# Performance work log

Hardware: AMD Instinct MI355X
Metric: run time of the kernel (lower is better)

The kernel has to match this reference:

```python
import jax, jax.numpy as jnp
import numpy as np

B, T, N = 256, 512, 256
START, STOP = 254, 255


def setup_inputs() -> dict:
    key = jax.random.key(0)
    k1, k2, k3 = jax.random.split(key, 3)
    inputs = jax.random.normal(k1, (B, T, N), dtype=jnp.float32)
    transitions = jax.random.normal(k2, (N, N), dtype=jnp.float32)
    # sentinel rows/cols as in __init__
    transitions = transitions.at[START, :].set(-10000.0).at[:, STOP].set(-10000.0)
    tags = jax.random.randint(k3, (B, T), 0, N, dtype=jnp.int32)
    mask = jnp.ones((B, T), dtype=jnp.int32)
    return {"inputs": inputs, "transitions": transitions, "tags": tags, "mask": mask}


def _input_likelihood(inputs, transitions, fmask):
    # alpha[b, tag]: log-sum over paths ending at tag
    alpha0 = transitions[:, START][None, :] + inputs[:, 0, :]

    def step(alpha, xs):
        emit, m = xs  # emit: (B, N), m: (B,)
        # inner[b, next, prev] = alpha[b, prev] + (emit[b, next] + trans[next, prev]) * mask[b, i-1]
        inner = alpha[:, None, :] + (emit[:, :, None] + transitions[None, :, :]) * m[:, None, None]
        return jax.nn.logsumexp(inner, axis=-1), None

    xs = (jnp.swapaxes(inputs[:, 1:, :], 0, 1), jnp.swapaxes(fmask[:, :-1], 0, 1))
    alpha, _ = jax.lax.scan(step, alpha0, xs)
    stops = alpha + transitions[STOP][None, :]
    return jax.nn.logsumexp(stops, axis=-1)  # (B,)


def _joint_likelihood(inputs, transitions, tags, fmask):
    score = transitions[tags[:, 0], START]  # (B,)
    # transitions[next, prev] * mask[:, i+1], summed over steps
    trans_sc = transitions[tags[:, 1:], tags[:, :-1]] * fmask[:, 1:]
    # inputs[b, i, prev_tag] * mask[:, i]
    emit_sc = jnp.take_along_axis(inputs[:, :-1, :], tags[:, :-1, None], axis=2)[..., 0] * fmask[:, :-1]
    score = score + trans_sc.sum(axis=-1) + emit_sc.sum(axis=-1)
    last_idx = (fmask.sum(axis=-1) - 1.0).astype(jnp.int32)  # (B,)
    last_tags = jnp.take_along_axis(tags, last_idx[:, None], axis=1)[:, 0]
    last_input = jnp.take_along_axis(inputs[:, -1, :], last_tags[:, None], axis=1)[:, 0]
    return score + transitions[STOP, last_tags] + last_input * fmask[:, -1]


def reference(inputs, transitions, tags, mask):
    fmask = mask.astype(jnp.float32)
    log_denominator = _input_likelihood(inputs, transitions, fmask)
    log_numerator = _joint_likelihood(inputs, transitions, tags, fmask)
    return jnp.sum(log_numerator - log_denominator)
```

## Files before the change

### kernel.cpp

```cpp
#include <hip/hip_runtime.h>
#include <hip/hip_bf16.h>
#include <stdint.h>

#define B_    256
#define T_    512
#define N_    256
#define START_ 254
#define STOP_  255
#define GCOLS 16
#define NF    16
#define ND    32
#define LOG2E 1.4426950408889634f
#define LN2   0.6931471805599453f

#define WSB_OFF 65536
#define WCF_OFF 131072
#define WCB_OFF 131328

typedef __attribute__((ext_vector_type(4))) float floatx4;
typedef __attribute__((ext_vector_type(4))) unsigned int uintx4;
typedef __attribute__((ext_vector_type(8))) int v8i;

template<bool X> struct BC { static constexpr bool value = X; };

__device__ __forceinline__ void lds_barrier() {
    asm volatile("s_waitcnt lgkmcnt(0)\n\ts_barrier" ::: "memory");
}

__device__ __forceinline__ int pk_fp8x4(float a, float b, float c, float d) {
    int r = __builtin_amdgcn_cvt_pk_fp8_f32(a, b, 0, false);
    return __builtin_amdgcn_cvt_pk_fp8_f32(c, d, r, true);
}
__device__ __forceinline__ int pk_bf8x4(float a, float b, float c, float d) {
    int r = __builtin_amdgcn_cvt_pk_bf8_f32(a, b, 0, false);
    return __builtin_amdgcn_cvt_pk_bf8_f32(c, d, r, true);
}

struct DenomShared {
    alignas(16) char  V[2][4096];
    alignas(16) float mbuf[GCOLS * 36];
    alignas(16) float sbuf[GCOLS * 20];
    int flag;
};

template<bool ISF>
__device__ __forceinline__ void denom_path(
    DenomShared& sh, const float* __restrict__ inputs,
    const float* __restrict__ trans, const int* __restrict__ mask,
    float* __restrict__ ws, int blkLocal)
{
    const int tid = threadIdx.x;
    const int w = tid >> 6;
    const int l = tid & 63;
    const int q = l >> 4;
    const int b = l & 15;
    const int bg = blkLocal * GCOLS + b;
    const int j0 = 32 * w + 4 * q;
    const int S = ISF ? 256 : 255;
    const int scl = 0x7F7F7F7F;

    auto EIDX = [](int s) { return ISF ? s : (511 - s); };
    auto MIDX = [](int s) { return ISF ? (s - 1) : (511 - s); };

    int wa[2];
    #pragma unroll
    for (int mt = 0; mt < 2; ++mt)
        wa[mt] = ((((2 * w + mt) >> 3) * 2 + mt) << 10)
               + ((w & 3) << 8) + (b << 4) + (q << 2);
    const int rbase = l << 4;

    v8i afrag[2][2];
    #pragma unroll
    for (int mt = 0; mt < 2; ++mt) {
        const int row = 32 * w + 16 * mt + b;
        #pragma unroll
        for (int c = 0; c < 2; ++c) {
            v8i a;
            #pragma unroll
            for (int g8 = 0; g8 < 8; ++g8) {
                float e[4];
                if (ISF) {
                    floatx4 t = *(const floatx4*)(trans + row * N_ + c * 128 + q * 32 + 4 * g8);
                    #pragma unroll
                    for (int ii = 0; ii < 4; ++ii)
                        e[ii] = __builtin_amdgcn_exp2f(t[ii] * LOG2E);
                } else {
                    #pragma unroll
                    for (int ii = 0; ii < 4; ++ii) {
                        const int k = c * 128 + q * 32 + 4 * g8 + ii;
                        e[ii] = __builtin_amdgcn_exp2f(trans[k * N_ + row] * LOG2E);
                    }
                }
                a[g8] = pk_fp8x4(e[0], e[1], e[2], e[3]);
            }
            afrag[mt][c] = a;
        }
    }

    {
        const int* mrow = mask + blkLocal * GCOLS * T_;
        bool hd = false;
        #pragma unroll
        for (int i = 0; i < GCOLS * T_ / 512; ++i)
            hd |= (mrow[tid + 512 * i] == 0);
        if (tid == 0) sh.flag = 0;
        __syncthreads();
        if (__any(hd) && l == 0) atomicOr(&sh.flag, 1);
        __syncthreads();
    }
    const bool anyDead = (sh.flag != 0);

    const float* emitp = inputs + (size_t)bg * T_ * N_;
    const int*   maskp = mask + bg * T_;
    float C = 0.f;
    float u[2][4];

    if (ISF) {
        #pragma unroll
        for (int mt = 0; mt < 2; ++mt) {
            floatx4 em = *(const floatx4*)(emitp + j0 + 16 * mt);
            #pragma unroll
            for (int r = 0; r < 4; ++r) {
                const int j = j0 + 16 * mt + r;
                u[mt][r] = __builtin_amdgcn_exp2f((trans[j * N_ + START_] + em[r]) * LOG2E);
            }
        }
    } else {
        #pragma unroll
        for (int mt = 0; mt < 2; ++mt) {
            floatx4 st = *(const floatx4*)(trans + STOP_ * N_ + j0 + 16 * mt);
            #pragma unroll
            for (int r = 0; r < 4; ++r)
                u[mt][r] = __builtin_amdgcn_exp2f(st[r] * LOG2E);
        }
    }
    {
        float mx = u[0][0], sm = 0.f;
        #pragma unroll
        for (int mt = 0; mt < 2; ++mt)
            #pragma unroll
            for (int r = 0; r < 4; ++r) { mx = fmaxf(mx, u[mt][r]); sm += u[mt][r]; }
        sh.mbuf[b * 36 + w * 4 + q] = mx;
        sm += __shfl_xor(sm, 32, 64);
        if (l < 32) sh.sbuf[b * 20 + w * 2 + q] = sm;

        float xpi[2][4] = {{1.f,1.f,1.f,1.f},{1.f,1.f,1.f,1.f}};
        if (!ISF) {
            #pragma unroll
            for (int mt = 0; mt < 2; ++mt) {
                floatx4 e = *(const floatx4*)(emitp + (size_t)511 * N_ + j0 + 16 * mt);
                #pragma unroll
                for (int r = 0; r < 4; ++r)
                    xpi[mt][r] = __builtin_amdgcn_exp2f(e[r] * LOG2E);
            }
        }
        #pragma unroll
        for (int mt = 0; mt < 2; ++mt)
            *(int*)(sh.V[0] + wa[mt]) =
                pk_bf8x4(u[mt][0] * xpi[mt][0], u[mt][1] * xpi[mt][1],
                         u[mt][2] * xpi[mt][2], u[mt][3] * xpi[mt][3]);
    }

    auto run = [&](auto fastc) {
        constexpr bool FAST = decltype(fastc)::value;
        floatx4 ebuf[2][2];
        float   mrot[2] = {1.f, 1.f};
        ebuf[0][0] = *(const floatx4*)(emitp + (size_t)EIDX(1) * N_ + j0);
        ebuf[0][1] = *(const floatx4*)(emitp + (size_t)EIDX(1) * N_ + j0 + 16);
        ebuf[1][0] = *(const floatx4*)(emitp + (size_t)EIDX(2) * N_ + j0);
        ebuf[1][1] = *(const floatx4*)(emitp + (size_t)EIDX(2) * N_ + j0 + 16);
        if (!FAST) {
            mrot[0] = (float)maskp[MIDX(1)];
            mrot[1] = (float)maskp[MIDX(2)];
        }
        lds_barrier();

        auto body = [&](int s, int pr, int cur) {
            const int sp = (s + 2 <= S) ? s + 2 : S;
            floatx4 eC0 = *(const floatx4*)(emitp + (size_t)EIDX(sp) * N_ + j0);
            floatx4 eC1 = *(const floatx4*)(emitp + (size_t)EIDX(sp) * N_ + j0 + 16);
            float mC = 1.f;
            if (!FAST) mC = (float)maskp[MIDX(sp)];

            const char* vb = sh.V[pr];
            v8i bfrag[2];
            #pragma unroll
            for (int c = 0; c < 2; ++c) {
                uintx4 r0 = *(const uintx4*)(vb + (c << 11) + rbase);
                uintx4 r1 = *(const uintx4*)(vb + (c << 11) + 1024 + rbase);
                v8i bf;
                bf[0] = r0[0]; bf[1] = r0[1]; bf[2] = r0[2]; bf[3] = r0[3];
                bf[4] = r1[0]; bf[5] = r1[1]; bf[6] = r1[2]; bf[7] = r1[3];
                bfrag[c] = bf;
            }

            const float* mb = &sh.mbuf[b * 36];
            float cmax;
            {
                floatx4 mm[8];
                #pragma unroll
                for (int i = 0; i < 8; ++i) mm[i] = *(const floatx4*)(mb + 4 * i);
                floatx4 mv = mm[0];
                #pragma unroll
                for (int i = 1; i < 8; ++i)
                    #pragma unroll
                    for (int r = 0; r < 4; ++r) mv[r] = fmaxf(mv[r], mm[i][r]);
                cmax = fmaxf(fmaxf(mv[0], mv[1]), fmaxf(mv[2], mv[3]));
            }
            const uint32_t cb = __builtin_bit_cast(uint32_t, cmax);
            const int eb = (int)((cb >> 23) & 0xFFu);
            const float rs = __builtin_bit_cast(float, (uint32_t)(249 - eb) << 23);
            const float dCf = (float)(122 - eb);

            float xpv[2][4];
            #pragma unroll
            for (int r = 0; r < 4; ++r) {
                if (ISF) {
                    xpv[0][r] = __builtin_amdgcn_exp2f(fmaf(ebuf[cur][0][r], LOG2E, dCf));
                    xpv[1][r] = __builtin_amdgcn_exp2f(fmaf(ebuf[cur][1][r], LOG2E, dCf));
                } else {
                    xpv[0][r] = __builtin_amdgcn_exp2f(ebuf[cur][0][r] * LOG2E);
                    xpv[1][r] = __builtin_amdgcn_exp2f(ebuf[cur][1][r] * LOG2E);
                }
            }

            floatx4 a0 = {0.f,0.f,0.f,0.f}, a1 = {0.f,0.f,0.f,0.f};
            a0 = __builtin_amdgcn_mfma_scale_f32_16x16x128_f8f6f4(
                     afrag[0][0], bfrag[0], a0, 0, 1, 0, scl, 0, scl);
            a1 = __builtin_amdgcn_mfma_scale_f32_16x16x128_f8f6f4(
                     afrag[1][0], bfrag[0], a1, 0, 1, 0, scl, 0, scl);
            a0 = __builtin_amdgcn_mfma_scale_f32_16x16x128_f8f6f4(
                     afrag[0][1], bfrag[1], a0, 0, 1, 0, scl, 0, scl);
            a1 = __builtin_amdgcn_mfma_scale_f32_16x16x128_f8f6f4(
                     afrag[1][1], bfrag[1], a1, 0, 1, 0, scl, 0, scl);

            if (FAST) {
                #pragma unroll
                for (int r = 0; r < 4; ++r) {
                    if (ISF) {
                        u[0][r] = a0[r] * xpv[0][r];
                        u[1][r] = a1[r] * xpv[1][r];
                    } else {
                        u[0][r] = a0[r] * rs;
                        u[1][r] = a1[r] * rs;
                    }
                }
            } else {
                const bool live = (mrot[cur] != 0.f);
                float csv = 0.f;
                if (__any(!live)) {
                    const float* sb = &sh.sbuf[b * 20];
                    floatx4 s0 = *(const floatx4*)sb,       s1 = *(const floatx4*)(sb + 4);
                    floatx4 s2 = *(const floatx4*)(sb + 8), s3 = *(const floatx4*)(sb + 12);
                    csv = ((((s0[0] + s0[1]) + (s0[2] + s0[3])) +
                            ((s1[0] + s1[1]) + (s1[2] + s1[3]))) +
                           (((s2[0] + s2[1]) + (s2[2] + s2[3])) +
                            ((s3[0] + s3[1]) + (s3[2] + s3[3])))) * rs;
                }
                #pragma unroll
                for (int r = 0; r < 4; ++r) {
                    if (ISF) {
                        u[0][r] = live ? a0[r] * xpv[0][r] : csv;
                        u[1][r] = live ? a1[r] * xpv[1][r] : csv;
                    } else {
                        u[0][r] = live ? a0[r] * rs : csv;
                        u[1][r] = live ? a1[r] * rs : csv;
                    }
                }
            }
            C += (float)(eb - 122);

            {
                float mx = fmaxf(fmaxf(fmaxf(u[0][0], u[0][1]), fmaxf(u[0][2], u[0][3])),
                                 fmaxf(fmaxf(u[1][0], u[1][1]), fmaxf(u[1][2], u[1][3])));
                sh.mbuf[b * 36 + w * 4 + q] = mx;
                if (!FAST) {
                    float sm = ((u[0][0] + u[0][1]) + (u[0][2] + u[0][3]))
                             + ((u[1][0] + u[1][1]) + (u[1][2] + u[1][3]));
                    sm += __shfl_xor(sm, 32, 64);
                    if (l < 32) sh.sbuf[b * 20 + w * 2 + q] = sm;
                }
            }
            #pragma unroll
            for (int mt = 0; mt < 2; ++mt) {
                *(int*)(sh.V[pr ^ 1] + wa[mt]) = ISF
                    ? pk_bf8x4(u[mt][0], u[mt][1], u[mt][2], u[mt][3])
                    : pk_bf8x4(u[mt][0] * xpv[mt][0], u[mt][1] * xpv[mt][1],
                               u[mt][2] * xpv[mt][2], u[mt][3] * xpv[mt][3]);
            }
            lds_barrier();
            ebuf[cur][0] = eC0; ebuf[cur][1] = eC1;
            if (!FAST) mrot[cur] = mC;
        };

        #pragma unroll 1
        for (int g = 0; g < 127; ++g) {
            body(2 * g + 1, 0, 0);
            body(2 * g + 2, 1, 1);
        }
        if (ISF) { body(255, 0, 0); body(256, 1, 1); }
        else     { body(255, 0, 0); }
    };

    if (anyDead) run(BC<false>{});
    else         run(BC<true>{});

    float* wsV = ws + (ISF ? 0 : WSB_OFF);
    #pragma unroll
    for (int mt = 0; mt < 2; ++mt) {
        floatx4 vv = {u[mt][0], u[mt][1], u[mt][2], u[mt][3]};
        *(floatx4*)&wsV[(size_t)bg * N_ + j0 + 16 * mt] = vv;
    }
    if (tid < 16) {
        float* wsC = ws + (ISF ? WCF_OFF : WCB_OFF);
        wsC[blkLocal * GCOLS + tid] = C;
    }
}

__global__ __launch_bounds__(512, 2) void crf_main(
    const float* __restrict__ inputs, const float* __restrict__ trans,
    const int* __restrict__ tags, const int* __restrict__ mask,
    float* __restrict__ out, float* __restrict__ ws)
{
    __shared__ DenomShared sh;

    if (blockIdx.x >= ND) {
        float* nred = sh.sbuf;
        int*   nredi = (int*)(sh.sbuf + 8);
        const int bb = blockIdx.x - ND;
        const int t  = threadIdx.x;
        const int tg = tags[bb * T_ + t];
        const float fm = (float)mask[bb * T_ + t];
        float part = 0.f;
        if (t >= 1)      part += trans[tg * N_ + tags[bb * T_ + t - 1]] * fm;
        if (t <= T_ - 2) part += inputs[((size_t)bb * T_ + t) * N_ + tg] * fm;
        int ms = mask[bb * T_ + t];
        #pragma unroll
        for (int off = 1; off < 64; off <<= 1) {
            part += __shfl_xor(part, off, 64);
            ms   += __shfl_xor(ms, off, 64);
        }
        if ((t & 63) == 0) { nred[t >> 6] = part; nredi[t >> 6] = ms; }
        __syncthreads();
        if (t == 0) {
            float tot = 0.f; int mtot = 0;
            for (int i = 0; i < 8; ++i) { tot += nred[i]; mtot += nredi[i]; }
            tot += trans[tags[bb * T_] * N_ + START_];
            const int last = mtot - 1;
            const int lt = tags[bb * T_ + last];
            tot += trans[STOP_ * N_ + lt]
                 + inputs[((size_t)bb * T_ + (T_ - 1)) * N_ + lt]
                   * (float)mask[bb * T_ + T_ - 1];
            atomicAdd(out, tot);
        }
        return;
    }

    if (blockIdx.x < NF) denom_path<true>(sh, inputs, trans, mask, ws, blockIdx.x);
    else                 denom_path<false>(sh, inputs, trans, mask, ws, blockIdx.x - NF);
}

__global__ __launch_bounds__(256) void crf_combine(
    const float* __restrict__ ws, float* __restrict__ out)
{
    __shared__ float red[4];
    const int bb = blockIdx.x;
    const int t = threadIdx.x;
    float p = ws[(size_t)bb * N_ + t] * ws[WSB_OFF + (size_t)bb * N_ + t];
    #pragma unroll
    for (int off = 1; off < 64; off <<= 1) p += __shfl_xor(p, off, 64);
    if ((t & 63) == 0) red[t >> 6] = p;
    __syncthreads();
    if (t == 0) {
        const float tot = red[0] + red[1] + red[2] + red[3];
        const float denom = (ws[WCF_OFF + bb] + ws[WCB_OFF + bb]
                             + __builtin_amdgcn_logf(tot)) * LN2;
        atomicAdd(out, -denom);
    }
}

extern "C" void kernel_launch(void* const* d_in, const int* in_sizes, int n_in,
                              void* d_out, int out_size, void* d_ws, size_t ws_size,
                              hipStream_t stream) {
    const float* inputs = (const float*)d_in[0];
    const float* trans  = (const float*)d_in[1];
    const int*   tags   = (const int*)d_in[2];
    const int*   mask   = (const int*)d_in[3];
    float* out = (float*)d_out;
    float* ws  = (float*)d_ws;
    hipMemsetAsync(out, 0, sizeof(float), stream);
    crf_main<<<dim3(ND + B_), dim3(512), 0, stream>>>(inputs, trans, tags, mask, out, ws);
    crf_combine<<<dim3(B_), dim3(256), 0, stream>>>(ws, out);
}
```

Before: 344.0 us.

## Precompute exp(inputs) as bf16 in a prepass and spread denominator over more blocks

Adds a parallel prepass kernel that computes exp(inputs) once and stores it as bf16 in the workspace. The serial recurrence then loads these half-size values instead of doing exp2 per step. It also cuts batch columns per denominator block from 16 to 4, so 128 blocks run the scan instead of 32. This uses more of the GPU for the latency-bound recurrence, at the cost of 12 of 16 column lanes per block doing dummy work. It also adds an extra full pass over the 128 MB input and brings bf16 precision risk, including possible underflow or overflow of exp values without the per-step scaling offset.

Result: slower. 356.4 us (+3.6%).

```diff
diff --git a/kernel.cpp b/kernel.cpp
--- a/kernel.cpp
+++ b/kernel.cpp
@@ -7,19 +7,22 @@
 #define N_    256
 #define START_ 254
 #define STOP_  255
-#define GCOLS 16
-#define NF    16
-#define ND    32
+#define GCOLS 4
+#define NF    64
+#define ND    128
 #define LOG2E 1.4426950408889634f
 #define LN2   0.6931471805599453f
 
 #define WSB_OFF 65536
 #define WCF_OFF 131072
 #define WCB_OFF 131328
+#define XP_BYTE_OFF ((size_t)1 << 20)
+#define WS_NEED (XP_BYTE_OFF + (size_t)B_ * T_ * N_ * 2)
 
 typedef __attribute__((ext_vector_type(4))) float floatx4;
 typedef __attribute__((ext_vector_type(4))) unsigned int uintx4;
 typedef __attribute__((ext_vector_type(8))) int v8i;
+typedef __attribute__((ext_vector_type(4))) unsigned short ushort4_t;
 
 template<bool X> struct BC { static constexpr bool value = X; };
 
@@ -27,6 +30,14 @@
     asm volatile("s_waitcnt lgkmcnt(0)\n\ts_barrier" ::: "memory");
 }
 
+__device__ __forceinline__ unsigned short f2bf(float f) {
+    uint32_t u = __builtin_bit_cast(uint32_t, f);
+    u = (u + 0x7FFFu + ((u >> 16) & 1u)) >> 16;
+    return (unsigned short)u;
+}
+__device__ __forceinline__ float bf2f(unsigned short h) {
+    return __builtin_bit_cast(float, (uint32_t)h << 16);
+}
 __device__ __forceinline__ int pk_fp8x4(float a, float b, float c, float d) {
     int r = __builtin_amdgcn_cvt_pk_fp8_f32(a, b, 0, false);
     return __builtin_amdgcn_cvt_pk_fp8_f32(c, d, r, true);
@@ -38,15 +49,16 @@
 
 struct DenomShared {
     alignas(16) char  V[2][4096];
-    alignas(16) float mbuf[GCOLS * 36];
-    alignas(16) float sbuf[GCOLS * 20];
+    alignas(16) float mbuf[16 * 36];
+    alignas(16) float sbuf[16 * 20];
     int flag;
 };
 
-template<bool ISF>
+template<bool ISF, bool PRE>
 __device__ __forceinline__ void denom_path(
     DenomShared& sh, const float* __restrict__ inputs,
     const float* __restrict__ trans, const int* __restrict__ mask,
+    const unsigned short* __restrict__ xp,
     float* __restrict__ ws, int blkLocal)
 {
     const int tid = threadIdx.x;
@@ -54,7 +66,8 @@
     const int l = tid & 63;
     const int q = l >> 4;
     const int b = l & 15;
-    const int bg = blkLocal * GCOLS + b;
+    const bool real = (b < GCOLS);
+    const int bgc = blkLocal * GCOLS + (real ? b : 0);
     const int j0 = 32 * w + 4 * q;
     const int S = ISF ? 256 : 255;
     const int scl = 0x7F7F7F7F;
@@ -110,21 +123,39 @@
     }
     const bool anyDead = (sh.flag != 0);
 
-    const float* emitp = inputs + (size_t)bg * T_ * N_;
-    const int*   maskp = mask + bg * T_;
+    const float* emitp = inputs + (size_t)bgc * T_ * N_;
+    const unsigned short* xprow = xp + (size_t)bgc * T_ * N_;
+    const int* maskp = mask + bgc * T_;
     float C = 0.f;
     float u[2][4];
 
     if (ISF) {
-        #pragma unroll
-        for (int mt = 0; mt < 2; ++mt) {
-            floatx4 em = *(const floatx4*)(emitp + j0 + 16 * mt);
+        float x0[2][4] = {};
+        if constexpr (PRE) {
+            if (real) {
+                ushort4_t h0 = *(const ushort4_t*)(xprow + j0);
+                ushort4_t h1 = *(const ushort4_t*)(xprow + j0 + 16);
+                #pragma unroll
+                for (int r = 0; r < 4; ++r) { x0[0][r] = bf2f(h0[r]); x0[1][r] = bf2f(h1[r]); }
+            }
+        } else {
+            if (real) {
+                floatx4 e0 = *(const floatx4*)(emitp + j0);
+                floatx4 e1 = *(const floatx4*)(emitp + j0 + 16);
+                #pragma unroll
+                for (int r = 0; r < 4; ++r) {
+                    x0[0][r] = __builtin_amdgcn_exp2f(e0[r] * LOG2E);
+                    x0[1][r] = __builtin_amdgcn_exp2f(e1[r] * LOG2E);
+                }
+            }
+        }
+        #pragma unroll
+        for (int mt = 0; mt < 2; ++mt)
             #pragma unroll
             for (int r = 0; r < 4; ++r) {
                 const int j = j0 + 16 * mt + r;
-                u[mt][r] = __builtin_amdgcn_exp2f((trans[j * N_ + START_] + em[r]) * LOG2E);
-            }
-        }
+                u[mt][r] = __builtin_amdgcn_exp2f(trans[j * N_ + START_] * LOG2E) * x0[mt][r];
+            }
     } else {
         #pragma unroll
         for (int mt = 0; mt < 2; ++mt) {
@@ -144,14 +175,30 @@
         sm += __shfl_xor(sm, 32, 64);
         if (l < 32) sh.sbuf[b * 20 + w * 2 + q] = sm;
 
-        float xpi[2][4] = {{1.f,1.f,1.f,1.f},{1.f,1.f,1.f,1.f}};
-        if (!ISF) {
-            #pragma unroll
-            for (int mt = 0; mt < 2; ++mt) {
-                floatx4 e = *(const floatx4*)(emitp + (size_t)511 * N_ + j0 + 16 * mt);
-                #pragma unroll
-                for (int r = 0; r < 4; ++r)
-                    xpi[mt][r] = __builtin_amdgcn_exp2f(e[r] * LOG2E);
+        float xpi[2][4] = {};
+        if (ISF) {
+            #pragma unroll
+            for (int mt = 0; mt < 2; ++mt)
+                #pragma unroll
+                for (int r = 0; r < 4; ++r) xpi[mt][r] = 1.f;
+        } else {
+            if constexpr (PRE) {
+                if (real) {
+                    ushort4_t h0 = *(const ushort4_t*)(xprow + (size_t)511 * N_ + j0);
+                    ushort4_t h1 = *(const ushort4_t*)(xprow + (size_t)511 * N_ + j0 + 16);
+                    #pragma unroll
+                    for (int r = 0; r < 4; ++r) { xpi[0][r] = bf2f(h0[r]); xpi[1][r] = bf2f(h1[r]); }
+                }
+            } else {
+                if (real) {
+                    floatx4 e0 = *(const floatx4*)(emitp + (size_t)511 * N_ + j0);
+                    floatx4 e1 = *(const floatx4*)(emitp + (size_t)511 * N_ + j0 + 16);
+                    #pragma unroll
+                    for (int r = 0; r < 4; ++r) {
+                        xpi[0][r] = __builtin_amdgcn_exp2f(e0[r] * LOG2E);
+                        xpi[1][r] = __builtin_amdgcn_exp2f(e1[r] * LOG2E);
+                    }
+                }
             }
         }
         #pragma unroll
@@ -163,22 +210,41 @@
 
     auto run = [&](auto fastc) {
         constexpr bool FAST = decltype(fastc)::value;
-        floatx4 ebuf[2][2];
-        float   mrot[2] = {1.f, 1.f};
-        ebuf[0][0] = *(const floatx4*)(emitp + (size_t)EIDX(1) * N_ + j0);
-        ebuf[0][1] = *(const floatx4*)(emitp + (size_t)EIDX(1) * N_ + j0 + 16);
-        ebuf[1][0] = *(const floatx4*)(emitp + (size_t)EIDX(2) * N_ + j0);
-        ebuf[1][1] = *(const floatx4*)(emitp + (size_t)EIDX(2) * N_ + j0 + 16);
-        if (!FAST) {
-            mrot[0] = (float)maskp[MIDX(1)];
-            mrot[1] = (float)maskp[MIDX(2)];
+        ushort4_t ebh[2][2] = {};
+        floatx4   ebf[2][2] = {};
+        float     mrot[2] = {1.f, 1.f};
+        #pragma unroll
+        for (int i = 0; i < 2; ++i) {
+            if constexpr (PRE) {
+                if (real) {
+                    ebh[i][0] = *(const ushort4_t*)(xprow + (size_t)EIDX(i + 1) * N_ + j0);
+                    ebh[i][1] = *(const ushort4_t*)(xprow + (size_t)EIDX(i + 1) * N_ + j0 + 16);
+                }
+            } else {
+                if (real) {
+                    ebf[i][0] = *(const floatx4*)(emitp + (size_t)EIDX(i + 1) * N_ + j0);
+                    ebf[i][1] = *(const floatx4*)(emitp + (size_t)EIDX(i + 1) * N_ + j0 + 16);
+                }
+            }
+            if (!FAST) mrot[i] = (float)maskp[MIDX(i + 1)];
         }
         lds_barrier();
 
         auto body = [&](int s, int pr, int cur) {
             const int sp = (s + 2 <= S) ? s + 2 : S;
-            floatx4 eC0 = *(const floatx4*)(emitp + (size_t)EIDX(sp) * N_ + j0);
-            floatx4 eC1 = *(const floatx4*)(emitp + (size_t)EIDX(sp) * N_ + j0 + 16);
+            ushort4_t hC0 = {}, hC1 = {};
+            floatx4   fC0 = {}, fC1 = {};
+            if constexpr (PRE) {
+                if (real) {
+                    hC0 = *(const ushort4_t*)(xprow + (size_t)EIDX(sp) * N_ + j0);
+                    hC1 = *(const ushort4_t*)(xprow + (size_t)EIDX(sp) * N_ + j0 + 16);
+                }
+            } else {
+                if (real) {
+                    fC0 = *(const floatx4*)(emitp + (size_t)EIDX(sp) * N_ + j0);
+                    fC1 = *(const floatx4*)(emitp + (size_t)EIDX(sp) * N_ + j0 + 16);
+                }
+            }
             float mC = 1.f;
             if (!FAST) mC = (float)maskp[MIDX(sp)];
 
@@ -213,14 +279,22 @@
             const float dCf = (float)(122 - eb);
 
             float xpv[2][4];
-            #pragma unroll
-            for (int r = 0; r < 4; ++r) {
-                if (ISF) {
-                    xpv[0][r] = __builtin_amdgcn_exp2f(fmaf(ebuf[cur][0][r], LOG2E, dCf));
-                    xpv[1][r] = __builtin_amdgcn_exp2f(fmaf(ebuf[cur][1][r], LOG2E, dCf));
-                } else {
-                    xpv[0][r] = __builtin_amdgcn_exp2f(ebuf[cur][0][r] * LOG2E);
-                    xpv[1][r] = __builtin_amdgcn_exp2f(ebuf[cur][1][r] * LOG2E);
+            if constexpr (PRE) {
+                #pragma unroll
+                for (int r = 0; r < 4; ++r) {
+                    xpv[0][r] = bf2f(ebh[cur][0][r]);
+                    xpv[1][r] = bf2f(ebh[cur][1][r]);
+                }
+            } else {
+                #pragma unroll
+                for (int r = 0; r < 4; ++r) {
+                    if (ISF) {
+                        xpv[0][r] = __builtin_amdgcn_exp2f(fmaf(ebf[cur][0][r], LOG2E, dCf));
+                        xpv[1][r] = __builtin_amdgcn_exp2f(fmaf(ebf[cur][1][r], LOG2E, dCf));
+                    } else {
+                        xpv[0][r] = __builtin_amdgcn_exp2f(ebf[cur][0][r] * LOG2E);
+                        xpv[1][r] = __builtin_amdgcn_exp2f(ebf[cur][1][r] * LOG2E);
+                    }
                 }
             }
 
@@ -238,8 +312,10 @@
                 #pragma unroll
                 for (int r = 0; r < 4; ++r) {
                     if (ISF) {
-                        u[0][r] = a0[r] * xpv[0][r];
-                        u[1][r] = a1[r] * xpv[1][r];
+                        if (PRE) { u[0][r] = (a0[r] * rs) * xpv[0][r];
+                                   u[1][r] = (a1[r] * rs) * xpv[1][r]; }
+                        else     { u[0][r] = a0[r] * xpv[0][r];
+                                   u[1][r] = a1[r] * xpv[1][r]; }
                     } else {
                         u[0][r] = a0[r] * rs;
                         u[1][r] = a1[r] * rs;
@@ -260,8 +336,10 @@
                 #pragma unroll
                 for (int r = 0; r < 4; ++r) {
                     if (ISF) {
-                        u[0][r] = live ? a0[r] * xpv[0][r] : csv;
-                        u[1][r] = live ? a1[r] * xpv[1][r] : csv;
+                        if (PRE) { u[0][r] = live ? (a0[r] * rs) * xpv[0][r] : csv;
+                                   u[1][r] = live ? (a1[r] * rs) * xpv[1][r] : csv; }
+                        else     { u[0][r] = live ? a0[r] * xpv[0][r] : csv;
+                                   u[1][r] = live ? a1[r] * xpv[1][r] : csv; }
                     } else {
                         u[0][r] = live ? a0[r] * rs : csv;
                         u[1][r] = live ? a1[r] * rs : csv;
@@ -289,7 +367,8 @@
                                u[mt][2] * xpv[mt][2], u[mt][3] * xpv[mt][3]);
             }
             lds_barrier();
-            ebuf[cur][0] = eC0; ebuf[cur][1] = eC1;
+            if constexpr (PRE) { ebh[cur][0] = hC0; ebh[cur][1] = hC1; }
+            else               { ebf[cur][0] = fC0; ebf[cur][1] = fC1; }
             if (!FAST) mrot[cur] = mC;
         };
 
@@ -305,22 +384,43 @@
     if (anyDead) run(BC<false>{});
     else         run(BC<true>{});
 
-    float* wsV = ws + (ISF ? 0 : WSB_OFF);
-    #pragma unroll
-    for (int mt = 0; mt < 2; ++mt) {
-        floatx4 vv = {u[mt][0], u[mt][1], u[mt][2], u[mt][3]};
-        *(floatx4*)&wsV[(size_t)bg * N_ + j0 + 16 * mt] = vv;
-    }
-    if (tid < 16) {
+    if (real) {
+        const int bg = blkLocal * GCOLS + b;
+        float* wsV = ws + (ISF ? 0 : WSB_OFF);
+        #pragma unroll
+        for (int mt = 0; mt < 2; ++mt) {
+            floatx4 vv = {u[mt][0], u[mt][1], u[mt][2], u[mt][3]};
+            *(floatx4*)&wsV[(size_t)bg * N_ + j0 + 16 * mt] = vv;
+        }
+    }
+    if (tid < GCOLS) {
         float* wsC = ws + (ISF ? WCF_OFF : WCB_OFF);
         wsC[blkLocal * GCOLS + tid] = C;
     }
 }
 
+__global__ __launch_bounds__(512) void crf_prepass(
+    const float* __restrict__ in, unsigned short* __restrict__ xp)
+{
+    const size_t total4 = (size_t)B_ * T_ * N_ / 4;
+    size_t i = (size_t)blockIdx.x * 512 + threadIdx.x;
+    const size_t stride = (size_t)gridDim.x * 512;
+    for (; i < total4; i += stride) {
+        floatx4 v = *(const floatx4*)(in + 4 * i);
+        ushort4_t o;
+        #pragma unroll
+        for (int r = 0; r < 4; ++r)
+            o[r] = f2bf(__builtin_amdgcn_exp2f(v[r] * LOG2E));
+        *(ushort4_t*)(xp + 4 * i) = o;
+    }
+}
+
+template<bool PRE>
 __global__ __launch_bounds__(512, 2) void crf_main(
     const float* __restrict__ inputs, const float* __restrict__ trans,
     const int* __restrict__ tags, const int* __restrict__ mask,
-    float* __restrict__ out, float* __restrict__ ws)
+    float* __restrict__ out, float* __restrict__ ws,
+    const unsigned short* __restrict__ xp)
 {
     __shared__ DenomShared sh;
 
@@ -356,8 +456,10 @@
         return;
     }
 
-    if (blockIdx.x < NF) denom_path<true>(sh, inputs, trans, mask, ws, blockIdx.x);
-    else                 denom_path<false>(sh, inputs, trans, mask, ws, blockIdx.x - NF);
+    if (blockIdx.x < NF)
+        denom_path<true,  PRE>(sh, inputs, trans, mask, xp, ws, blockIdx.x);
+    else
+        denom_path<false, PRE>(sh, inputs, trans, mask, xp, ws, blockIdx.x - NF);
 }
 
 __global__ __launch_bounds__(256) void crf_combine(
@@ -388,7 +490,15 @@
     const int*   mask   = (const int*)d_in[3];
     float* out = (float*)d_out;
     float* ws  = (float*)d_ws;
+    unsigned short* xp = (unsigned short*)((char*)d_ws + XP_BYTE_OFF);
     hipMemsetAsync(out, 0, sizeof(float), stream);
-    crf_main<<<dim3(ND + B_), dim3(512), 0, stream>>>(inputs, trans, tags, mask, out, ws);
+    if (ws_size >= WS_NEED) {
+        crf_prepass<<<dim3(4096), dim3(512), 0, stream>>>(inputs, xp);
+        crf_main<true><<<dim3(ND + B_), dim3(512), 0, stream>>>(
+            inputs, trans, tags, mask, out, ws, xp);
+    } else {
+        crf_main<false><<<dim3(ND + B_), dim3(512), 0, stream>>>(
+            inputs, trans, tags, mask, out, ws, xp);
+    }
     crf_combine<<<dim3(B_), dim3(256), 0, stream>>>(ws, out);
 }
```

## Spread denominator recursion over more blocks with fewer batch columns each

Applied to the files above, without the earlier changes.

Cuts the batch columns handled per denominator block from 16 to 4, so 128 blocks instead of 32 run the serial recursion. MFMA tiles stay 16 wide, so the unused lanes are padded with zero emissions. Each step's max reduction now reads packed fp16 values from LDS and reduces them with packed half max, which shortens the per-step critical path. The intent is to fill more CUs and make each serial step cheaper. The cost is wasted MFMA work on padding, more total blocks, and some risk from the lower precision of the scale exponent.

New measurement: 386.8 us. 1.12x slower.

```diff
diff --git a/kernel.cpp b/kernel.cpp
--- a/kernel.cpp
+++ b/kernel.cpp
@@ -7,9 +7,9 @@
 #define N_    256
 #define START_ 254
 #define STOP_  255
-#define GCOLS 16
-#define NF    16
-#define ND    32
+#define GCOLS 4
+#define NF    64
+#define ND    128
 #define LOG2E 1.4426950408889634f
 #define LN2   0.6931471805599453f
 
@@ -20,6 +20,7 @@
 typedef __attribute__((ext_vector_type(4))) float floatx4;
 typedef __attribute__((ext_vector_type(4))) unsigned int uintx4;
 typedef __attribute__((ext_vector_type(8))) int v8i;
+typedef _Float16 h2 __attribute__((ext_vector_type(2)));
 
 template<bool X> struct BC { static constexpr bool value = X; };
 
@@ -35,11 +36,15 @@
     int r = __builtin_amdgcn_cvt_pk_bf8_f32(a, b, 0, false);
     return __builtin_amdgcn_cvt_pk_bf8_f32(c, d, r, true);
 }
+__device__ __forceinline__ h2 h2max(h2 a, h2 b) {
+    return __builtin_elementwise_max(a, b);
+}
+__device__ __forceinline__ h2 ash2(unsigned x) { return __builtin_bit_cast(h2, x); }
 
 struct DenomShared {
     alignas(16) char  V[2][4096];
-    alignas(16) float mbuf[GCOLS * 36];
-    alignas(16) float sbuf[GCOLS * 20];
+    alignas(16) unsigned short mexp[16 * 40];
+    alignas(16) float sbuf[16 * 20];
     int flag;
 };
 
@@ -54,7 +59,8 @@
     const int l = tid & 63;
     const int q = l >> 4;
     const int b = l & 15;
-    const int bg = blkLocal * GCOLS + b;
+    const bool real = (b < GCOLS);
+    const int bgc = blkLocal * GCOLS + (real ? b : 0);
     const int j0 = 32 * w + 4 * q;
     const int S = ISF ? 256 : 255;
     const int scl = 0x7F7F7F7F;
@@ -110,21 +116,29 @@
     }
     const bool anyDead = (sh.flag != 0);
 
-    const float* emitp = inputs + (size_t)bg * T_ * N_;
-    const int*   maskp = mask + bg * T_;
+    const float* emitp = inputs + (size_t)bgc * T_ * N_;
+    const int* maskp = mask + bgc * T_;
     float C = 0.f;
     float u[2][4];
 
     if (ISF) {
-        #pragma unroll
-        for (int mt = 0; mt < 2; ++mt) {
-            floatx4 em = *(const floatx4*)(emitp + j0 + 16 * mt);
+        float x0[2][4] = {};
+        if (real) {
+            floatx4 e0 = *(const floatx4*)(emitp + j0);
+            floatx4 e1 = *(const floatx4*)(emitp + j0 + 16);
+            #pragma unroll
+            for (int r = 0; r < 4; ++r) {
+                x0[0][r] = __builtin_amdgcn_exp2f(e0[r] * LOG2E);
+                x0[1][r] = __builtin_amdgcn_exp2f(e1[r] * LOG2E);
+            }
+        }
+        #pragma unroll
+        for (int mt = 0; mt < 2; ++mt)
             #pragma unroll
             for (int r = 0; r < 4; ++r) {
                 const int j = j0 + 16 * mt + r;
-                u[mt][r] = __builtin_amdgcn_exp2f((trans[j * N_ + START_] + em[r]) * LOG2E);
-            }
-        }
+                u[mt][r] = __builtin_amdgcn_exp2f(trans[j * N_ + START_] * LOG2E) * x0[mt][r];
+            }
     } else {
         #pragma unroll
         for (int mt = 0; mt < 2; ++mt) {
@@ -140,18 +154,23 @@
         for (int mt = 0; mt < 2; ++mt)
             #pragma unroll
             for (int r = 0; r < 4; ++r) { mx = fmaxf(mx, u[mt][r]); sm += u[mt][r]; }
-        sh.mbuf[b * 36 + w * 4 + q] = mx;
+        sh.mexp[b * 40 + w * 4 + q] = __builtin_bit_cast(unsigned short, (_Float16)mx);
         sm += __shfl_xor(sm, 32, 64);
         if (l < 32) sh.sbuf[b * 20 + w * 2 + q] = sm;
 
-        float xpi[2][4] = {{1.f,1.f,1.f,1.f},{1.f,1.f,1.f,1.f}};
-        if (!ISF) {
-            #pragma unroll
-            for (int mt = 0; mt < 2; ++mt) {
-                floatx4 e = *(const floatx4*)(emitp + (size_t)511 * N_ + j0 + 16 * mt);
+        float xpi[2][4] = {};
+        if (ISF) {
+            #pragma unroll
+            for (int mt = 0; mt < 2; ++mt)
                 #pragma unroll
-                for (int r = 0; r < 4; ++r)
-                    xpi[mt][r] = __builtin_amdgcn_exp2f(e[r] * LOG2E);
+                for (int r = 0; r < 4; ++r) xpi[mt][r] = 1.f;
+        } else if (real) {
+            floatx4 e0 = *(const floatx4*)(emitp + (size_t)511 * N_ + j0);
+            floatx4 e1 = *(const floatx4*)(emitp + (size_t)511 * N_ + j0 + 16);
+            #pragma unroll
+            for (int r = 0; r < 4; ++r) {
+                xpi[0][r] = __builtin_amdgcn_exp2f(e0[r] * LOG2E);
+                xpi[1][r] = __builtin_amdgcn_exp2f(e1[r] * LOG2E);
             }
         }
         #pragma unroll
@@ -163,22 +182,25 @@
 
     auto run = [&](auto fastc) {
         constexpr bool FAST = decltype(fastc)::value;
-        floatx4 ebuf[2][2];
+        floatx4 ebf[2][2] = {};
         float   mrot[2] = {1.f, 1.f};
-        ebuf[0][0] = *(const floatx4*)(emitp + (size_t)EIDX(1) * N_ + j0);
-        ebuf[0][1] = *(const floatx4*)(emitp + (size_t)EIDX(1) * N_ + j0 + 16);
-        ebuf[1][0] = *(const floatx4*)(emitp + (size_t)EIDX(2) * N_ + j0);
-        ebuf[1][1] = *(const floatx4*)(emitp + (size_t)EIDX(2) * N_ + j0 + 16);
-        if (!FAST) {
-            mrot[0] = (float)maskp[MIDX(1)];
-            mrot[1] = (float)maskp[MIDX(2)];
+        #pragma unroll
+        for (int i = 0; i < 2; ++i) {
+            if (real) {
+                ebf[i][0] = *(const floatx4*)(emitp + (size_t)EIDX(i + 1) * N_ + j0);
+                ebf[i][1] = *(const floatx4*)(emitp + (size_t)EIDX(i + 1) * N_ + j0 + 16);
+            }
+            if (!FAST) mrot[i] = (float)maskp[MIDX(i + 1)];
         }
         lds_barrier();
 
         auto body = [&](int s, int pr, int cur) {
             const int sp = (s + 2 <= S) ? s + 2 : S;
-            floatx4 eC0 = *(const floatx4*)(emitp + (size_t)EIDX(sp) * N_ + j0);
-            floatx4 eC1 = *(const floatx4*)(emitp + (size_t)EIDX(sp) * N_ + j0 + 16);
+            floatx4 fC0 = {}, fC1 = {};
+            if (real) {
+                fC0 = *(const floatx4*)(emitp + (size_t)EIDX(sp) * N_ + j0);
+                fC1 = *(const floatx4*)(emitp + (size_t)EIDX(sp) * N_ + j0 + 16);
+            }
             float mC = 1.f;
             if (!FAST) mC = (float)maskp[MIDX(sp)];
 
@@ -194,21 +216,16 @@
                 bfrag[c] = bf;
             }
 
-            const float* mb = &sh.mbuf[b * 36];
-            float cmax;
-            {
-                floatx4 mm[8];
-                #pragma unroll
-                for (int i = 0; i < 8; ++i) mm[i] = *(const floatx4*)(mb + 4 * i);
-                floatx4 mv = mm[0];
-                #pragma unroll
-                for (int i = 1; i < 8; ++i)
-                    #pragma unroll
-                    for (int r = 0; r < 4; ++r) mv[r] = fmaxf(mv[r], mm[i][r]);
-                cmax = fmaxf(fmaxf(mv[0], mv[1]), fmaxf(mv[2], mv[3]));
-            }
-            const uint32_t cb = __builtin_bit_cast(uint32_t, cmax);
-            const int eb = (int)((cb >> 23) & 0xFFu);
+            const uintx4* mp = (const uintx4*)&sh.mexp[b * 40];
+            uintx4 q0 = mp[0], q1 = mp[1], q2 = mp[2], q3 = mp[3];
+            h2 hm = ash2(q0[0]);
+            hm = h2max(hm, ash2(q0[1])); hm = h2max(hm, ash2(q0[2])); hm = h2max(hm, ash2(q0[3]));
+            hm = h2max(hm, ash2(q1[0])); hm = h2max(hm, ash2(q1[1])); hm = h2max(hm, ash2(q1[2])); hm = h2max(hm, ash2(q1[3]));
+            hm = h2max(hm, ash2(q2[0])); hm = h2max(hm, ash2(q2[1])); hm = h2max(hm, ash2(q2[2])); hm = h2max(hm, ash2(q2[3]));
+            hm = h2max(hm, ash2(q3[0])); hm = h2max(hm, ash2(q3[1])); hm = h2max(hm, ash2(q3[2])); hm = h2max(hm, ash2(q3[3]));
+            const _Float16 fmx = hm[0] > hm[1] ? hm[0] : hm[1];
+            const unsigned short mbits = __builtin_bit_cast(unsigned short, fmx);
+            const int eb = (int)((mbits >> 10) & 0x1F) + 112;
             const float rs = __builtin_bit_cast(float, (uint32_t)(249 - eb) << 23);
             const float dCf = (float)(122 - eb);
 
@@ -216,11 +233,11 @@
             #pragma unroll
             for (int r = 0; r < 4; ++r) {
                 if (ISF) {
-                    xpv[0][r] = __builtin_amdgcn_exp2f(fmaf(ebuf[cur][0][r], LOG2E, dCf));
-                    xpv[1][r] = __builtin_amdgcn_exp2f(fmaf(ebuf[cur][1][r], LOG2E, dCf));
+                    xpv[0][r] = __builtin_amdgcn_exp2f(fmaf(ebf[cur][0][r], LOG2E, dCf));
+                    xpv[1][r] = __builtin_amdgcn_exp2f(fmaf(ebf[cur][1][r], LOG2E, dCf));
                 } else {
-                    xpv[0][r] = __builtin_amdgcn_exp2f(ebuf[cur][0][r] * LOG2E);
-                    xpv[1][r] = __builtin_amdgcn_exp2f(ebuf[cur][1][r] * LOG2E);
+                    xpv[0][r] = __builtin_amdgcn_exp2f(ebf[cur][0][r] * LOG2E);
+                    xpv[1][r] = __builtin_amdgcn_exp2f(ebf[cur][1][r] * LOG2E);
                 }
             }
 
@@ -273,7 +290,7 @@
             {
                 float mx = fmaxf(fmaxf(fmaxf(u[0][0], u[0][1]), fmaxf(u[0][2], u[0][3])),
                                  fmaxf(fmaxf(u[1][0], u[1][1]), fmaxf(u[1][2], u[1][3])));
-                sh.mbuf[b * 36 + w * 4 + q] = mx;
+                sh.mexp[b * 40 + w * 4 + q] = __builtin_bit_cast(unsigned short, (_Float16)mx);
                 if (!FAST) {
                     float sm = ((u[0][0] + u[0][1]) + (u[0][2] + u[0][3]))
                              + ((u[1][0] + u[1][1]) + (u[1][2] + u[1][3]));
@@ -289,7 +306,7 @@
                                u[mt][2] * xpv[mt][2], u[mt][3] * xpv[mt][3]);
             }
             lds_barrier();
-            ebuf[cur][0] = eC0; ebuf[cur][1] = eC1;
+            ebf[cur][0] = fC0; ebf[cur][1] = fC1;
             if (!FAST) mrot[cur] = mC;
         };
 
@@ -305,13 +322,16 @@
     if (anyDead) run(BC<false>{});
     else         run(BC<true>{});
 
-    float* wsV = ws + (ISF ? 0 : WSB_OFF);
-    #pragma unroll
-    for (int mt = 0; mt < 2; ++mt) {
-        floatx4 vv = {u[mt][0], u[mt][1], u[mt][2], u[mt][3]};
-        *(floatx4*)&wsV[(size_t)bg * N_ + j0 + 16 * mt] = vv;
-    }
-    if (tid < 16) {
+    if (real) {
+        const int bg = blkLocal * GCOLS + b;
+        float* wsV = ws + (ISF ? 0 : WSB_OFF);
+        #pragma unroll
+        for (int mt = 0; mt < 2; ++mt) {
+            floatx4 vv = {u[mt][0], u[mt][1], u[mt][2], u[mt][3]};
+            *(floatx4*)&wsV[(size_t)bg * N_ + j0 + 16 * mt] = vv;
+        }
+    }
+    if (tid < GCOLS) {
         float* wsC = ws + (ISF ? WCF_OFF : WCB_OFF);
         wsC[blkLocal * GCOLS + tid] = C;
     }
@@ -356,8 +376,10 @@
         return;
     }
 
-    if (blockIdx.x < NF) denom_path<true>(sh, inputs, trans, mask, ws, blockIdx.x);
-    else                 denom_path<false>(sh, inputs, trans, mask, ws, blockIdx.x - NF);
+    if (blockIdx.x < NF)
+        denom_path<true >(sh, inputs, trans, mask, ws, blockIdx.x);
+    else
+        denom_path<false>(sh, inputs, trans, mask, ws, blockIdx.x - NF);
 }
 
 __global__ __launch_bounds__(256) void crf_combine(
```
